# Performance work log

Measured on AMD Instinct MI355X. Metric: run time of the kernel, lower is better.

## Reference

```python
import jax, jax.numpy as jnp
import numpy as np

DIM = 512
HEADS = 8
DIM_HEAD = 64
INNER = HEADS * DIM_HEAD  # 512
EPS = 1e-6


def setup_inputs() -> dict:
    key = jax.random.key(0)
    ks = jax.random.split(key, 6)
    B, N = 8, 2048
    x = jax.random.normal(ks[0], (B, N, DIM), dtype=jnp.float32)
    # nn.Linear stores weight as [out, in]; we keep that layout and transpose in matmul.
    w_qkv = jax.random.normal(ks[1], (3 * INNER, DIM), dtype=jnp.float32) * (1.0 / np.sqrt(DIM))
    w_proj = jax.random.normal(ks[2], (DIM, INNER), dtype=jnp.float32) * (1.0 / np.sqrt(INNER))
    b_proj = jax.random.normal(ks[3], (DIM,), dtype=jnp.float32) * 0.01
    ln_gamma = jnp.ones((DIM,), dtype=jnp.float32)
    ln_beta = jnp.zeros((DIM,), dtype=jnp.float32)
    return {"x": x, "w_qkv": w_qkv, "w_proj": w_proj, "b_proj": b_proj,
            "ln_gamma": ln_gamma, "ln_beta": ln_beta}


def reference(x, w_qkv, w_proj, b_proj, ln_gamma, ln_beta):
    B, N, D = x.shape
    H, Dh = HEADS, DIM_HEAD
    # LayerNorm (eps=1e-6)
    mu = jnp.mean(x, axis=-1, keepdims=True)
    var = jnp.mean(jnp.square(x - mu), axis=-1, keepdims=True)
    xn = (x - mu) * jax.lax.rsqrt(var + EPS) * ln_gamma + ln_beta
    # QKV projection (no bias)
    qkv = xn @ w_qkv.T  # [B, N, 3*INNER]
    q, k, v = jnp.split(qkv, 3, axis=-1)
    # [B, N, H, Dh] -> [B, H, N, Dh]
    q = q.reshape(B, N, H, Dh).transpose(0, 2, 1, 3)
    k = k.reshape(B, N, H, Dh).transpose(0, 2, 1, 3)
    v = v.reshape(B, N, H, Dh).transpose(0, 2, 1, 3)
    scale = Dh ** (-0.5)
    attn = jnp.einsum('bhnd,bhmd->bhnm', q, k) * scale  # [B, H, N, N]
    attn = jax.nn.softmax(attn, axis=-1)
    out = jnp.einsum('bhnm,bhmd->bhnd', attn, v)  # [B, H, N, Dh]
    out = out.transpose(0, 2, 1, 3).reshape(B, N, H * Dh)
    out = out @ w_proj.T + b_proj
    return out
```

## Files before the change

kernel.cpp:

```cpp
#include <hip/hip_runtime.h>

typedef unsigned short u16;
typedef __bf16 bf16x8 __attribute__((ext_vector_type(8)));
typedef float f32x4 __attribute__((ext_vector_type(4)));
typedef float f32x16 __attribute__((ext_vector_type(16)));

#define DIMD 512
#define SEQN 2048
#define NB   8
#define NH   8
#define DH   64
#define BHN  (NB*NH)
#define MROWS (NB*SEQN)
#define QSCALE 0.18033688f

__device__ __forceinline__ u16 f2bf(float f) {
  union { float f; unsigned u; } x; x.f = f;
  unsigned r = x.u + 0x7fffu + ((x.u >> 16) & 1u);
  return (u16)(r >> 16);
}

__device__ __forceinline__ void gll16(const u16* g, u16* lbase) {
#if __has_builtin(__builtin_amdgcn_global_load_lds)
  __builtin_amdgcn_global_load_lds(
      (const __attribute__((address_space(1))) unsigned int*)g,
      (__attribute__((address_space(3))) unsigned int*)lbase, 16, 0, 0);
#else
  *(uint4*)((u16*)lbase + (threadIdx.x & 63) * 8) = *(const uint4*)g;
#endif
}

__device__ __forceinline__ bf16x8 mkfrag(float e0, float e1, float e2, float e3,
                                          float e4, float e5, float e6, float e7) {
  unsigned a0, a1, a2, a3;
  asm("v_cvt_pk_bf16_f32 %0, %1, %2" : "=v"(a0) : "v"(e0), "v"(e1));
  asm("v_cvt_pk_bf16_f32 %0, %1, %2" : "=v"(a1) : "v"(e2), "v"(e3));
  asm("v_cvt_pk_bf16_f32 %0, %1, %2" : "=v"(a2) : "v"(e4), "v"(e5));
  asm("v_cvt_pk_bf16_f32 %0, %1, %2" : "=v"(a3) : "v"(e6), "v"(e7));
  asm volatile("v_permlane32_swap_b32 %0, %1" : "+v"(a0), "+v"(a2));
  asm volatile("v_permlane32_swap_b32 %0, %1" : "+v"(a1), "+v"(a3));
  union { unsigned u[4]; bf16x8 v; } r;
  r.u[0] = a0; r.u[1] = a1; r.u[2] = a2; r.u[3] = a3;
  return r.v;
}

__global__ __launch_bounds__(256) void wcvt2(
    const float* __restrict__ wa, const float* __restrict__ wb,
    u16* __restrict__ oa, u16* __restrict__ ob, int na, int nb) {
  int i = (blockIdx.x * 256 + threadIdx.x) * 8;
  const float* src; u16* dst; int idx;
  if (i < na) { src = wa; dst = oa; idx = i; }
  else { idx = i - na; if (idx >= nb) return; src = wb; dst = ob; }
  float4 f0 = *(const float4*)(src + idx);
  float4 f1 = *(const float4*)(src + idx + 4);
  union { uint4 v; u16 s[8]; } u;
  u.s[0] = f2bf(f0.x); u.s[1] = f2bf(f0.y); u.s[2] = f2bf(f0.z); u.s[3] = f2bf(f0.w);
  u.s[4] = f2bf(f1.x); u.s[5] = f2bf(f1.y); u.s[6] = f2bf(f1.z); u.s[7] = f2bf(f1.w);
  *(uint4*)(dst + idx) = u.v;
}

__global__ __launch_bounds__(256) void ln_kernel(
    const float* __restrict__ x, const float* __restrict__ gamma,
    const float* __restrict__ beta, u16* __restrict__ xn) {
  int row = blockIdx.x * 4 + (threadIdx.x >> 6);
  int lane = threadIdx.x & 63;
  const float* xr = x + (size_t)row * DIMD;
  float f[8], g[8], b[8];
  *(float4*)&f[0] = *(const float4*)(xr + lane * 8);
  *(float4*)&f[4] = *(const float4*)(xr + lane * 8 + 4);
  *(float4*)&g[0] = *(const float4*)(gamma + lane * 8);
  *(float4*)&g[4] = *(const float4*)(gamma + lane * 8 + 4);
  *(float4*)&b[0] = *(const float4*)(beta + lane * 8);
  *(float4*)&b[4] = *(const float4*)(beta + lane * 8 + 4);
  float sum = 0.f, sq = 0.f;
#pragma unroll
  for (int i = 0; i < 8; ++i) { sum += f[i]; sq += f[i] * f[i]; }
#pragma unroll
  for (int off = 1; off < 64; off <<= 1) {
    sum += __shfl_xor(sum, off, 64);
    sq  += __shfl_xor(sq, off, 64);
  }
  float mean = sum * (1.0f / DIMD);
  float var = sq * (1.0f / DIMD) - mean * mean;
  float rstd = rsqrtf(var + 1e-6f);
  union { uint4 v; u16 s[8]; } uo;
#pragma unroll
  for (int i = 0; i < 8; ++i)
    uo.s[i] = f2bf((f[i] - mean) * rstd * g[i] + b[i]);
  *(uint4*)(xn + (size_t)row * DIMD + lane * 8) = uo.v;
}

__global__ __launch_bounds__(256) void qkv_gemm(
    const u16* __restrict__ A, const u16* __restrict__ Bm,
    u16* __restrict__ qo, u16* __restrict__ ko, u16* __restrict__ vto) {
  __shared__ __align__(16) u16 la[128 * 64];
  __shared__ __align__(16) u16 lb[128 * 64];
  const int K = DIMD;
  int tid = threadIdx.x;
  int bm = blockIdx.x, bn = blockIdx.y;
  int wid = tid >> 6, lane = tid & 63, lm = lane & 15, quad = lane >> 4;
  int wm = wid >> 1, wn = wid & 1;
  int lsw = lm & 7;
  int part = bn >> 2;
  f32x4 acc[4][4] = {};
  const u16* Ab = A + (size_t)(bm * 128) * K;
  const u16* Bb = Bm + (size_t)(bn * 128) * K;
  int cb_row = lane >> 3, cb_sub = lane & 7;
  int xsrc = (cb_sub ^ cb_row) * 8;
  for (int k0 = 0; k0 < K; k0 += 64) {
    __syncthreads();
#pragma unroll
    for (int r = 0; r < 4; ++r) {
      int seg = wid * 4 + r;
      int row = seg * 8 + cb_row;
      size_t goff = (size_t)row * K + k0 + xsrc;
      gll16(Ab + goff, &la[seg * 512]);
      gll16(Bb + goff, &lb[seg * 512]);
    }
    __syncthreads();
#pragma unroll
    for (int h = 0; h < 2; ++h) {
      bf16x8 af[4], bfr[4];
#pragma unroll
      for (int i = 0; i < 4; ++i)
        af[i] = *(const bf16x8*)&la[(wm * 64 + i * 16 + lm) * 64 + (((h * 4 + quad) ^ lsw) * 8)];
#pragma unroll
      for (int j = 0; j < 4; ++j)
        bfr[j] = *(const bf16x8*)&lb[(wn * 64 + j * 16 + lm) * 64 + (((h * 4 + quad) ^ lsw) * 8)];
      if (part == 2) {
#pragma unroll
        for (int i = 0; i < 4; ++i)
#pragma unroll
          for (int j = 0; j < 4; ++j)
            acc[i][j] = __builtin_amdgcn_mfma_f32_16x16x32_bf16(af[i], bfr[j], acc[i][j], 0, 0, 0);
      } else {
#pragma unroll
        for (int i = 0; i < 4; ++i)
#pragma unroll
          for (int j = 0; j < 4; ++j)
            acc[i][j] = __builtin_amdgcn_mfma_f32_16x16x32_bf16(bfr[j], af[i], acc[i][j], 0, 0, 0);
      }
    }
  }
  if (part == 2) {
#pragma unroll
    for (int i = 0; i < 4; ++i)
#pragma unroll
      for (int j = 0; j < 4; ++j) {
        int col = bn * 128 + wn * 64 + j * 16 + lm;
        int rem = col & 511, h = rem >> 6, d = rem & 63;
        int rg = bm * 128 + wm * 64 + i * 16 + quad * 4;
        int b = rg >> 11, nn = rg & 2047;
        union { unsigned long long ll; u16 s4[4]; } pk;
#pragma unroll
        for (int r = 0; r < 4; ++r) pk.s4[r] = f2bf(acc[i][j][r]);
        *(unsigned long long*)&vto[((size_t)(b * NH + h) * DH + d) * SEQN + nn] = pk.ll;
      }
  } else {
    u16* dst = part ? ko : qo;
    float sc = part ? 1.0f : QSCALE;
#pragma unroll
    for (int i = 0; i < 4; ++i)
#pragma unroll
      for (int j = 0; j < 4; ++j) {
        int rg = bm * 128 + wm * 64 + i * 16 + lm;
        int b = rg >> 11, nn = rg & 2047;
        int col = bn * 128 + wn * 64 + j * 16 + quad * 4;
        int rem = col & 511, hh = rem >> 6, d = rem & 63;
        union { unsigned long long ll; __bf16 h4[4]; } pk;
#pragma unroll
        for (int r = 0; r < 4; ++r) pk.h4[r] = (__bf16)(acc[i][j][r] * sc);
        *(unsigned long long*)&dst[((size_t)(b * NH + hh) * SEQN + nn) * DH + d] = pk.ll;
      }
  }
}

__global__ __launch_bounds__(256, 2) void attn_kernel(
    const u16* __restrict__ q, const u16* __restrict__ k,
    const u16* __restrict__ vt, u16* __restrict__ att) {
  __shared__ __align__(16) u16 kt[2][64 * 64];
  __shared__ __align__(16) u16 vtt[2][64 * 64];
  int bh = blockIdx.x;
  int wid = threadIdx.x >> 6, lane = threadIdx.x & 63;
  int l31 = lane & 31, hi = lane >> 5;
  int qrow0 = blockIdx.y * 256 + wid * 64;
  const u16* qb = q + (size_t)bh * SEQN * DH;
  const u16* kb = k + (size_t)bh * SEQN * DH;
  const u16* vb = vt + (size_t)bh * DH * SEQN;

  int cb_row = lane >> 3, cb_sub = lane & 7;
  int xstage = (cb_sub ^ cb_row) * 8;

  bf16x8 qfA[4], qfB[4];
#pragma unroll
  for (int c = 0; c < 4; ++c) {
    qfA[c] = *(const bf16x8*)(qb + (size_t)(qrow0 + l31) * DH + c * 16 + hi * 8);
    qfB[c] = *(const bf16x8*)(qb + (size_t)(qrow0 + 32 + l31) * DH + c * 16 + hi * 8);
  }

  f32x16 OtA0 = {}, OtA1 = {}, OtB0 = {}, OtB1 = {};
  float lA = 0.f, lB = 0.f;

  auto stage = [&](int bsel, int j0) {
    if (wid < 2) {
#pragma unroll
      for (int i = 0; i < 4; ++i) {
        int seg = wid * 4 + i;
        int row = seg * 8 + cb_row;
        gll16(kb + (size_t)(j0 + row) * DH + xstage, &kt[bsel][seg * 512]);
      }
    } else {
#pragma unroll
      for (int i = 0; i < 4; ++i) {
        int seg = (wid - 2) * 4 + i;
        int row = seg * 8 + cb_row;
        gll16(vb + (size_t)row * SEQN + j0 + xstage, &vtt[bsel][seg * 512]);
      }
    }
  };

  stage(0, 0);
  for (int t = 0; t < SEQN / 64; ++t) {
    int bsel = t & 1;
    __syncthreads();
    if (t + 1 < SEQN / 64) stage(bsel ^ 1, (t + 1) * 64);

    bf16x8 pbA[4], pbB[4];
    int rsw = l31 & 7;
#pragma unroll
    for (int tb = 0; tb < 2; ++tb) {
      int row = tb * 32 + l31;
      f32x16 zA = {}, zB = {};
      __builtin_amdgcn_s_setprio(1);
#pragma unroll
      for (int c = 0; c < 4; ++c) {
        bf16x8 kf = *(const bf16x8*)&kt[bsel][row * 64 + (((2 * c + hi) ^ rsw) * 8)];
        zA = __builtin_amdgcn_mfma_f32_32x32x16_bf16(kf, qfA[c], zA, 0, 0, 0);
        zB = __builtin_amdgcn_mfma_f32_32x32x16_bf16(kf, qfB[c], zB, 0, 0, 0);
      }
      __builtin_amdgcn_s_setprio(0);
      float eA[16], eB[16];
#pragma unroll
      for (int r = 0; r < 16; ++r) {
        eA[r] = __builtin_amdgcn_exp2f(zA[r]); lA += eA[r];
        eB[r] = __builtin_amdgcn_exp2f(zB[r]); lB += eB[r];
      }
      pbA[tb * 2 + 0] = mkfrag(eA[0], eA[1], eA[2], eA[3], eA[4], eA[5], eA[6], eA[7]);
      pbA[tb * 2 + 1] = mkfrag(eA[8], eA[9], eA[10], eA[11], eA[12], eA[13], eA[14], eA[15]);
      pbB[tb * 2 + 0] = mkfrag(eB[0], eB[1], eB[2], eB[3], eB[4], eB[5], eB[6], eB[7]);
      pbB[tb * 2 + 1] = mkfrag(eB[8], eB[9], eB[10], eB[11], eB[12], eB[13], eB[14], eB[15]);
    }
#pragma unroll
    for (int c = 0; c < 4; ++c) {
      bf16x8 va0 = *(const bf16x8*)&vtt[bsel][l31 * 64 + (((2 * c + hi) ^ rsw) * 8)];
      bf16x8 va1 = *(const bf16x8*)&vtt[bsel][(32 + l31) * 64 + (((2 * c + hi) ^ rsw) * 8)];
      __builtin_amdgcn_s_setprio(1);
      OtA0 = __builtin_amdgcn_mfma_f32_32x32x16_bf16(va0, pbA[c], OtA0, 0, 0, 0);
      OtA1 = __builtin_amdgcn_mfma_f32_32x32x16_bf16(va1, pbA[c], OtA1, 0, 0, 0);
      OtB0 = __builtin_amdgcn_mfma_f32_32x32x16_bf16(va0, pbB[c], OtB0, 0, 0, 0);
      OtB1 = __builtin_amdgcn_mfma_f32_32x32x16_bf16(va1, pbB[c], OtB1, 0, 0, 0);
      __builtin_amdgcn_s_setprio(0);
    }
  }
  int b = bh >> 3, h = bh & 7;
  float lAf = lA + __shfl_xor(lA, 32, 64);
  float lBf = lB + __shfl_xor(lB, 32, 64);
  float invA = __builtin_amdgcn_rcpf(lAf);
  float invB = __builtin_amdgcn_rcpf(lBf);
  size_t rowA = ((size_t)(b * SEQN + qrow0 + l31)) * DIMD + h * DH;
  size_t rowB = ((size_t)(b * SEQN + qrow0 + 32 + l31)) * DIMD + h * DH;
#pragma unroll
  for (int rb = 0; rb < 4; ++rb) {
    union { unsigned long long ll; __bf16 h4[4]; } a0, a1, b0, b1;
#pragma unroll
    for (int rr = 0; rr < 4; ++rr) {
      a0.h4[rr] = (__bf16)(OtA0[rb * 4 + rr] * invA);
      a1.h4[rr] = (__bf16)(OtA1[rb * 4 + rr] * invA);
      b0.h4[rr] = (__bf16)(OtB0[rb * 4 + rr] * invB);
      b1.h4[rr] = (__bf16)(OtB1[rb * 4 + rr] * invB);
    }
    *(unsigned long long*)&att[rowA + rb * 8 + hi * 4] = a0.ll;
    *(unsigned long long*)&att[rowA + 32 + rb * 8 + hi * 4] = a1.ll;
    *(unsigned long long*)&att[rowB + rb * 8 + hi * 4] = b0.ll;
    *(unsigned long long*)&att[rowB + 32 + rb * 8 + hi * 4] = b1.ll;
  }
}

__global__ __launch_bounds__(256) void proj_gemm(
    const u16* __restrict__ A, const u16* __restrict__ Bm,
    const float* __restrict__ bias, float* __restrict__ C) {
  __shared__ __align__(16) u16 la[128 * 64];
  __shared__ __align__(16) u16 lb[128 * 64];
  const int K = DIMD, N = DIMD;
  int tid = threadIdx.x;
  int bm = blockIdx.x, bn = blockIdx.y;
  int wid = tid >> 6, lane = tid & 63, lm = lane & 15, quad = lane >> 4;
  int wm = wid >> 1, wn = wid & 1;
  int lsw = lm & 7;
  f32x4 acc[4][4] = {};
  const u16* Ab = A + (size_t)(bm * 128) * K;
  const u16* Bb = Bm + (size_t)(bn * 128) * K;
  int cb_row = lane >> 3, cb_sub = lane & 7;
  int xsrc = (cb_sub ^ cb_row) * 8;
  for (int k0 = 0; k0 < K; k0 += 64) {
    __syncthreads();
#pragma unroll
    for (int r = 0; r < 4; ++r) {
      int seg = wid * 4 + r;
      int row = seg * 8 + cb_row;
      size_t goff = (size_t)row * K + k0 + xsrc;
      gll16(Ab + goff, &la[seg * 512]);
      gll16(Bb + goff, &lb[seg * 512]);
    }
    __syncthreads();
#pragma unroll
    for (int h = 0; h < 2; ++h) {
      bf16x8 af[4], bfr[4];
#pragma unroll
      for (int i = 0; i < 4; ++i)
        af[i] = *(const bf16x8*)&la[(wm * 64 + i * 16 + lm) * 64 + (((h * 4 + quad) ^ lsw) * 8)];
#pragma unroll
      for (int j = 0; j < 4; ++j)
        bfr[j] = *(const bf16x8*)&lb[(wn * 64 + j * 16 + lm) * 64 + (((h * 4 + quad) ^ lsw) * 8)];
#pragma unroll
      for (int i = 0; i < 4; ++i)
#pragma unroll
        for (int j = 0; j < 4; ++j)
          acc[i][j] = __builtin_amdgcn_mfma_f32_16x16x32_bf16(bfr[j], af[i], acc[i][j], 0, 0, 0);
    }
  }
#pragma unroll
  for (int i = 0; i < 4; ++i)
#pragma unroll
    for (int j = 0; j < 4; ++j) {
      int rg = bm * 128 + wm * 64 + i * 16 + lm;
      int col = bn * 128 + wn * 64 + j * 16 + quad * 4;
      float4 bv = *(const float4*)(bias + col);
      float4 o;
      o.x = acc[i][j][0] + bv.x; o.y = acc[i][j][1] + bv.y;
      o.z = acc[i][j][2] + bv.z; o.w = acc[i][j][3] + bv.w;
      *(float4*)&C[(size_t)rg * N + col] = o;
    }
}

extern "C" void kernel_launch(void* const* d_in, const int* in_sizes, int n_in,
                              void* d_out, int out_size, void* d_ws, size_t ws_size,
                              hipStream_t stream) {
  const float* x      = (const float*)d_in[0];
  const float* w_qkv  = (const float*)d_in[1];
  const float* w_proj = (const float*)d_in[2];
  const float* b_proj = (const float*)d_in[3];
  const float* gamma  = (const float*)d_in[4];
  const float* beta   = (const float*)d_in[5];
  float* out = (float*)d_out;

  const size_t SZ = (size_t)MROWS * DIMD;
  u16* xn  = (u16*)d_ws;
  u16* q   = xn + SZ;
  u16* kk  = q + SZ;
  u16* vt  = kk + SZ;
  u16* wqb = vt + SZ;
  u16* wpb = wqb + (size_t)3 * DIMD * DIMD;
  u16* att = xn;

  const int NQKV = 3 * DIMD * DIMD;
  const int NPRJ = DIMD * DIMD;
  wcvt2<<<dim3((NQKV + NPRJ) / 2048), dim3(256), 0, stream>>>(
      w_qkv, w_proj, wqb, wpb, NQKV, NPRJ);
  ln_kernel<<<dim3(MROWS / 4), dim3(256), 0, stream>>>(x, gamma, beta, xn);
  qkv_gemm<<<dim3(MROWS / 128, (3 * DIMD) / 128), dim3(256), 0, stream>>>(
      xn, wqb, q, kk, vt);
  attn_kernel<<<dim3(BHN, SEQN / 256), dim3(256), 0, stream>>>(q, kk, vt, att);
  proj_gemm<<<dim3(MROWS / 128, DIMD / 128), dim3(256), 0, stream>>>(
      att, wpb, b_proj, out);
}
```

Measured before the change: 220.4 us.

## Software-pipeline attention loop: QK of next tile overlaps PV of previous, 4-stage LDS ring

```diff
diff --git a/kernel.cpp b/kernel.cpp
--- a/kernel.cpp
+++ b/kernel.cpp
@@ -43,6 +43,11 @@
   r.u[0] = a0; r.u[1] = a1; r.u[2] = a2; r.u[3] = a3;
   return r.v;
 }
+
+#define WAITV(N) asm volatile("s_waitcnt vmcnt(" #N ")" ::: "memory")
+#define BARRIER() do { asm volatile("" ::: "memory"); \
+                       __builtin_amdgcn_s_barrier();  \
+                       asm volatile("" ::: "memory"); } while (0)
 
 __global__ __launch_bounds__(256) void wcvt2(
     const float* __restrict__ wa, const float* __restrict__ wb,
@@ -178,8 +183,8 @@
 __global__ __launch_bounds__(256, 2) void attn_kernel(
     const u16* __restrict__ q, const u16* __restrict__ k,
     const u16* __restrict__ vt, u16* __restrict__ att) {
-  __shared__ __align__(16) u16 kt[2][64 * 64];
-  __shared__ __align__(16) u16 vtt[2][64 * 64];
+  __shared__ __align__(16) u16 kt[4][64 * 64];
+  __shared__ __align__(16) u16 vtt[4][64 * 64];
   int bh = blockIdx.x;
   int wid = threadIdx.x >> 6, lane = threadIdx.x & 63;
   int l31 = lane & 31, hi = lane >> 5;
@@ -190,6 +195,7 @@
 
   int cb_row = lane >> 3, cb_sub = lane & 7;
   int xstage = (cb_sub ^ cb_row) * 8;
+  int rsw = l31 & 7;
 
   bf16x8 qfA[4], qfB[4];
 #pragma unroll
@@ -199,9 +205,10 @@
   }
 
   f32x16 OtA0 = {}, OtA1 = {}, OtB0 = {}, OtB1 = {};
-  float lA = 0.f, lB = 0.f;
-
-  auto stage = [&](int bsel, int j0) {
+  f32x4 lAv = {}, lBv = {};
+
+  auto stage = [&](int t) {
+    int bsel = t & 3, j0 = t * 64;
     if (wid < 2) {
 #pragma unroll
       for (int i = 0; i < 4; ++i) {
@@ -219,52 +226,71 @@
     }
   };
 
-  stage(0, 0);
-  for (int t = 0; t < SEQN / 64; ++t) {
-    int bsel = t & 1;
-    __syncthreads();
-    if (t + 1 < SEQN / 64) stage(bsel ^ 1, (t + 1) * 64);
-
-    bf16x8 pbA[4], pbB[4];
-    int rsw = l31 & 7;
-#pragma unroll
-    for (int tb = 0; tb < 2; ++tb) {
-      int row = tb * 32 + l31;
-      f32x16 zA = {}, zB = {};
-      __builtin_amdgcn_s_setprio(1);
-#pragma unroll
-      for (int c = 0; c < 4; ++c) {
-        bf16x8 kf = *(const bf16x8*)&kt[bsel][row * 64 + (((2 * c + hi) ^ rsw) * 8)];
-        zA = __builtin_amdgcn_mfma_f32_32x32x16_bf16(kf, qfA[c], zA, 0, 0, 0);
-        zB = __builtin_amdgcn_mfma_f32_32x32x16_bf16(kf, qfB[c], zB, 0, 0, 0);
-      }
-      __builtin_amdgcn_s_setprio(0);
-      float eA[16], eB[16];
-#pragma unroll
-      for (int r = 0; r < 16; ++r) {
-        eA[r] = __builtin_amdgcn_exp2f(zA[r]); lA += eA[r];
-        eB[r] = __builtin_amdgcn_exp2f(zB[r]); lB += eB[r];
-      }
-      pbA[tb * 2 + 0] = mkfrag(eA[0], eA[1], eA[2], eA[3], eA[4], eA[5], eA[6], eA[7]);
-      pbA[tb * 2 + 1] = mkfrag(eA[8], eA[9], eA[10], eA[11], eA[12], eA[13], eA[14], eA[15]);
-      pbB[tb * 2 + 0] = mkfrag(eB[0], eB[1], eB[2], eB[3], eB[4], eB[5], eB[6], eB[7]);
-      pbB[tb * 2 + 1] = mkfrag(eB[8], eB[9], eB[10], eB[11], eB[12], eB[13], eB[14], eB[15]);
-    }
+  auto qk_tile = [&](int bsel, int tb, bf16x8* pA, bf16x8* pB,
+                     float* eA, float* eB) {
+    int row = tb * 32 + l31;
+    f32x16 zA = {}, zB = {};
+    __builtin_amdgcn_s_setprio(1);
 #pragma unroll
     for (int c = 0; c < 4; ++c) {
-      bf16x8 va0 = *(const bf16x8*)&vtt[bsel][l31 * 64 + (((2 * c + hi) ^ rsw) * 8)];
-      bf16x8 va1 = *(const bf16x8*)&vtt[bsel][(32 + l31) * 64 + (((2 * c + hi) ^ rsw) * 8)];
-      __builtin_amdgcn_s_setprio(1);
-      OtA0 = __builtin_amdgcn_mfma_f32_32x32x16_bf16(va0, pbA[c], OtA0, 0, 0, 0);
-      OtA1 = __builtin_amdgcn_mfma_f32_32x32x16_bf16(va1, pbA[c], OtA1, 0, 0, 0);
-      OtB0 = __builtin_amdgcn_mfma_f32_32x32x16_bf16(va0, pbB[c], OtB0, 0, 0, 0);
-      OtB1 = __builtin_amdgcn_mfma_f32_32x32x16_bf16(va1, pbB[c], OtB1, 0, 0, 0);
-      __builtin_amdgcn_s_setprio(0);
-    }
-  }
+      bf16x8 kf = *(const bf16x8*)&kt[bsel][row * 64 + (((2 * c + hi) ^ rsw) * 8)];
+      zA = __builtin_amdgcn_mfma_f32_32x32x16_bf16(kf, qfA[c], zA, 0, 0, 0);
+      zB = __builtin_amdgcn_mfma_f32_32x32x16_bf16(kf, qfB[c], zB, 0, 0, 0);
+    }
+    __builtin_amdgcn_s_setprio(0);
+#pragma unroll
+    for (int r = 0; r < 16; ++r) {
+      eA[r] = __builtin_amdgcn_exp2f(zA[r]); lAv[r & 3] += eA[r];
+      eB[r] = __builtin_amdgcn_exp2f(zB[r]); lBv[r & 3] += eB[r];
+    }
+    pA[0] = mkfrag(eA[0], eA[1], eA[2], eA[3], eA[4], eA[5], eA[6], eA[7]);
+    pA[1] = mkfrag(eA[8], eA[9], eA[10], eA[11], eA[12], eA[13], eA[14], eA[15]);
+    pB[0] = mkfrag(eB[0], eB[1], eB[2], eB[3], eB[4], eB[5], eB[6], eB[7]);
+    pB[1] = mkfrag(eB[8], eB[9], eB[10], eB[11], eB[12], eB[13], eB[14], eB[15]);
+  };
+
+  auto pv_half = [&](int vsel, int c0, bf16x8* pA, bf16x8* pB) {
+#pragma unroll
+    for (int c = c0; c < c0 + 2; ++c) {
+      bf16x8 va0 = *(const bf16x8*)&vtt[vsel][l31 * 64 + (((2 * c + hi) ^ rsw) * 8)];
+      bf16x8 va1 = *(const bf16x8*)&vtt[vsel][(32 + l31) * 64 + (((2 * c + hi) ^ rsw) * 8)];
+      OtA0 = __builtin_amdgcn_mfma_f32_32x32x16_bf16(va0, pA[c], OtA0, 0, 0, 0);
+      OtA1 = __builtin_amdgcn_mfma_f32_32x32x16_bf16(va1, pA[c], OtA1, 0, 0, 0);
+      OtB0 = __builtin_amdgcn_mfma_f32_32x32x16_bf16(va0, pB[c], OtB0, 0, 0, 0);
+      OtB1 = __builtin_amdgcn_mfma_f32_32x32x16_bf16(va1, pB[c], OtB1, 0, 0, 0);
+    }
+  };
+
+  bf16x8 pPA[4], pPB[4];
+  bf16x8 pCA[4], pCB[4];
+  float eA[16], eB[16];
+
+  stage(0); stage(1); stage(2);
+  WAITV(8);
+  BARRIER();
+  qk_tile(0, 0, &pPA[0], &pPB[0], eA, eB);
+  qk_tile(0, 1, &pPA[2], &pPB[2], eA, eB);
+
+  for (int t = 1; t < SEQN / 64; ++t) {
+    if (t < 31) { WAITV(4); } else { WAITV(0); }
+    BARRIER();
+    if (t <= 29) stage(t + 2);
+    int bsel = t & 3, vsel = (t - 1) & 3;
+    qk_tile(bsel, 0, &pCA[0], &pCB[0], eA, eB);
+    pv_half(vsel, 0, pPA, pPB);
+    qk_tile(bsel, 1, &pCA[2], &pCB[2], eA, eB);
+    pv_half(vsel, 2, pPA, pPB);
+#pragma unroll
+    for (int i = 0; i < 4; ++i) { pPA[i] = pCA[i]; pPB[i] = pCB[i]; }
+  }
+  pv_half(3, 0, pPA, pPB);
+  pv_half(3, 2, pPA, pPB);
+
   int b = bh >> 3, h = bh & 7;
-  float lAf = lA + __shfl_xor(lA, 32, 64);
-  float lBf = lB + __shfl_xor(lB, 32, 64);
+  float lAf = (lAv[0] + lAv[1]) + (lAv[2] + lAv[3]);
+  float lBf = (lBv[0] + lBv[1]) + (lBv[2] + lBv[3]);
+  lAf += __shfl_xor(lAf, 32, 64);
+  lBf += __shfl_xor(lBf, 32, 64);
   float invA = __builtin_amdgcn_rcpf(lAf);
   float invB = __builtin_amdgcn_rcpf(lBf);
   size_t rowA = ((size_t)(b * SEQN + qrow0 + l31)) * DIMD + h * DH;
```

Measured after the change: 223.1 us. No clear change (+1.2%).

## Double-buffer LDS tiles in QKV and projection GEMMs to overlap loads

Applied to the files above, without the earlier changes.

```diff
diff --git a/kernel.cpp b/kernel.cpp
--- a/kernel.cpp
+++ b/kernel.cpp
@@ -43,6 +43,11 @@
   r.u[0] = a0; r.u[1] = a1; r.u[2] = a2; r.u[3] = a3;
   return r.v;
 }
+
+#define WAITV(N) asm volatile("s_waitcnt vmcnt(" #N ")" ::: "memory")
+#define BARRIER() do { asm volatile("" ::: "memory"); \
+                       __builtin_amdgcn_s_barrier();  \
+                       asm volatile("" ::: "memory"); } while (0)
 
 __global__ __launch_bounds__(256) void wcvt2(
     const float* __restrict__ wa, const float* __restrict__ wb,
@@ -93,8 +98,8 @@
 __global__ __launch_bounds__(256) void qkv_gemm(
     const u16* __restrict__ A, const u16* __restrict__ Bm,
     u16* __restrict__ qo, u16* __restrict__ ko, u16* __restrict__ vto) {
-  __shared__ __align__(16) u16 la[128 * 64];
-  __shared__ __align__(16) u16 lb[128 * 64];
+  __shared__ __align__(16) u16 la[2][128 * 64];
+  __shared__ __align__(16) u16 lb[2][128 * 64];
   const int K = DIMD;
   int tid = threadIdx.x;
   int bm = blockIdx.x, bn = blockIdx.y;
@@ -107,26 +112,34 @@
   const u16* Bb = Bm + (size_t)(bn * 128) * K;
   int cb_row = lane >> 3, cb_sub = lane & 7;
   int xsrc = (cb_sub ^ cb_row) * 8;
-  for (int k0 = 0; k0 < K; k0 += 64) {
-    __syncthreads();
+
+  auto stage = [&](int ks) {
+    int bsel = ks & 1, k0 = ks * 64;
 #pragma unroll
     for (int r = 0; r < 4; ++r) {
       int seg = wid * 4 + r;
       int row = seg * 8 + cb_row;
       size_t goff = (size_t)row * K + k0 + xsrc;
-      gll16(Ab + goff, &la[seg * 512]);
-      gll16(Bb + goff, &lb[seg * 512]);
-    }
-    __syncthreads();
+      gll16(Ab + goff, &la[bsel][seg * 512]);
+      gll16(Bb + goff, &lb[bsel][seg * 512]);
+    }
+  };
+
+  stage(0);
+  for (int ks = 0; ks < 8; ++ks) {
+    BARRIER();
+    if (ks < 7) { stage(ks + 1); WAITV(8); } else { WAITV(0); }
+    BARRIER();
+    int bsel = ks & 1;
 #pragma unroll
     for (int h = 0; h < 2; ++h) {
       bf16x8 af[4], bfr[4];
 #pragma unroll
       for (int i = 0; i < 4; ++i)
-        af[i] = *(const bf16x8*)&la[(wm * 64 + i * 16 + lm) * 64 + (((h * 4 + quad) ^ lsw) * 8)];
+        af[i] = *(const bf16x8*)&la[bsel][(wm * 64 + i * 16 + lm) * 64 + (((h * 4 + quad) ^ lsw) * 8)];
 #pragma unroll
       for (int j = 0; j < 4; ++j)
-        bfr[j] = *(const bf16x8*)&lb[(wn * 64 + j * 16 + lm) * 64 + (((h * 4 + quad) ^ lsw) * 8)];
+        bfr[j] = *(const bf16x8*)&lb[bsel][(wn * 64 + j * 16 + lm) * 64 + (((h * 4 + quad) ^ lsw) * 8)];
       if (part == 2) {
 #pragma unroll
         for (int i = 0; i < 4; ++i)
@@ -289,8 +302,8 @@
 __global__ __launch_bounds__(256) void proj_gemm(
     const u16* __restrict__ A, const u16* __restrict__ Bm,
     const float* __restrict__ bias, float* __restrict__ C) {
-  __shared__ __align__(16) u16 la[128 * 64];
-  __shared__ __align__(16) u16 lb[128 * 64];
+  __shared__ __align__(16) u16 la[2][128 * 64];
+  __shared__ __align__(16) u16 lb[2][128 * 64];
   const int K = DIMD, N = DIMD;
   int tid = threadIdx.x;
   int bm = blockIdx.x, bn = blockIdx.y;
@@ -302,26 +315,34 @@
   const u16* Bb = Bm + (size_t)(bn * 128) * K;
   int cb_row = lane >> 3, cb_sub = lane & 7;
   int xsrc = (cb_sub ^ cb_row) * 8;
-  for (int k0 = 0; k0 < K; k0 += 64) {
-    __syncthreads();
+
+  auto stage = [&](int ks) {
+    int bsel = ks & 1, k0 = ks * 64;
 #pragma unroll
     for (int r = 0; r < 4; ++r) {
       int seg = wid * 4 + r;
       int row = seg * 8 + cb_row;
       size_t goff = (size_t)row * K + k0 + xsrc;
-      gll16(Ab + goff, &la[seg * 512]);
-      gll16(Bb + goff, &lb[seg * 512]);
-    }
-    __syncthreads();
+      gll16(Ab + goff, &la[bsel][seg * 512]);
+      gll16(Bb + goff, &lb[bsel][seg * 512]);
+    }
+  };
+
+  stage(0);
+  for (int ks = 0; ks < 8; ++ks) {
+    BARRIER();
+    if (ks < 7) { stage(ks + 1); WAITV(8); } else { WAITV(0); }
+    BARRIER();
+    int bsel = ks & 1;
 #pragma unroll
     for (int h = 0; h < 2; ++h) {
       bf16x8 af[4], bfr[4];
 #pragma unroll
       for (int i = 0; i < 4; ++i)
-        af[i] = *(const bf16x8*)&la[(wm * 64 + i * 16 + lm) * 64 + (((h * 4 + quad) ^ lsw) * 8)];
+        af[i] = *(const bf16x8*)&la[bsel][(wm * 64 + i * 16 + lm) * 64 + (((h * 4 + quad) ^ lsw) * 8)];
 #pragma unroll
       for (int j = 0; j < 4; ++j)
-        bfr[j] = *(const bf16x8*)&lb[(wn * 64 + j * 16 + lm) * 64 + (((h * 4 + quad) ^ lsw) * 8)];
+        bfr[j] = *(const bf16x8*)&lb[bsel][(wn * 64 + j * 16 + lm) * 64 + (((h * 4 + quad) ^ lsw) * 8)];
 #pragma unroll
       for (int i = 0; i < 4; ++i)
 #pragma unroll
```

Result: no change. 218.1 us (-1.0%).
